# Performance work log

Hardware: AMD Instinct MI355X
Metric: run time of the kernel (lower is better)

## Reference

```python
import jax, jax.numpy as jnp
import numpy as np

B, T, D, H, MLP, WIN = 4, 2048, 768, 12, 3072, 256
HD = D // H


def setup_inputs() -> dict:
    key = jax.random.key(0)
    ks = jax.random.split(key, 9)
    s = 0.02
    return {
        "x": jax.random.normal(ks[0], (B, T, D), jnp.float32),
        "in_proj_w": jax.random.normal(ks[1], (3 * D, D), jnp.float32) * s,
        "in_proj_b": jax.random.normal(ks[2], (3 * D,), jnp.float32) * s,
        "out_w": jax.random.normal(ks[3], (D, D), jnp.float32) * s,
        "out_b": jax.random.normal(ks[4], (D,), jnp.float32) * s,
        "w1": jax.random.normal(ks[5], (MLP, D), jnp.float32) * s,
        "b1": jax.random.normal(ks[6], (MLP,), jnp.float32) * s,
        "w2": jax.random.normal(ks[7], (D, MLP), jnp.float32) * s,
        "b2": jax.random.normal(ks[8], (D,), jnp.float32) * s,
        "ln1_g": jnp.ones((D,), jnp.float32),
        "ln1_b": jnp.zeros((D,), jnp.float32),
        "ln2_g": jnp.ones((D,), jnp.float32),
        "ln2_b": jnp.zeros((D,), jnp.float32),
        "window_size": WIN,
    }


def _layernorm(v, g, b, eps=1e-5):
    m = v.mean(-1, keepdims=True)
    var = ((v - m) ** 2).mean(-1, keepdims=True)
    return (v - m) / jnp.sqrt(var + eps) * g + b


def reference(x, in_proj_w, in_proj_b, out_w, out_b, w1, b1, w2, b2,
              ln1_g, ln1_b, ln2_g, ln2_b, window_size):
    Bx, Tx, Dx = x.shape
    # --- local (banded) multi-head self-attention on norm1(x) ---
    xn = _layernorm(x, ln1_g, ln1_b)
    qkv = xn @ in_proj_w.T + in_proj_b            # [B,T,3D]
    q, k, v = jnp.split(qkv, 3, axis=-1)
    to_heads = lambda t: t.reshape(Bx, Tx, H, HD).transpose(0, 2, 1, 3)  # [B,H,T,hd]
    q, k, v = to_heads(q), to_heads(k), to_heads(v)
    scale = jnp.asarray(1.0 / np.sqrt(HD), x.dtype)
    scores = jnp.einsum('bhqd,bhkd->bhqk', q, k) * scale  # [B,H,T,T]
    idx = jnp.arange(Tx)
    banned = jnp.abs(idx[:, None] - idx[None, :]) > window_size  # True = masked
    scores = jnp.where(banned, -jnp.inf, scores)
    attn = jax.nn.softmax(scores, axis=-1)
    o = jnp.einsum('bhqk,bhkd->bhqd', attn, v)
    o = o.transpose(0, 2, 1, 3).reshape(Bx, Tx, Dx)
    o = o @ out_w.T + out_b
    x = x + o
    # --- MLP block on norm2(x) ---
    xn = _layernorm(x, ln2_g, ln2_b)
    h = jax.nn.gelu(xn @ w1.T + b1, approximate=False)
    x = x + (h @ w2.T + b2)
    return x
```

## Files before the change

### kernel.cpp

```cpp
#include <hip/hip_runtime.h>
#include <hip/hip_bf16.h>

typedef __bf16 bf16;
typedef __bf16 v8bf __attribute__((ext_vector_type(8)));
typedef __bf16 v4bf __attribute__((ext_vector_type(4)));
typedef float  v4f  __attribute__((ext_vector_type(4)));

#define DEVI __device__ __forceinline__

constexpr int Bc   = 4;
constexpr int Tc   = 2048;
constexpr int Dc   = 768;
constexpr int Hc   = 12;
constexpr int HDc  = 64;
constexpr int MLPc = 3072;
constexpr int QKVc = 2304;
constexpr int BTc  = Bc * Tc;

DEVI float b2f(bf16 x) { return (float)x; }
DEVI bf16  f2b(float x) { return (bf16)x; }

#define GLDS(gp, lp) __builtin_amdgcn_global_load_lds( \
    (const __attribute__((address_space(1))) void*)(gp), \
    (__attribute__((address_space(3))) void*)(lp), 16, 0, 0)

__global__ __launch_bounds__(256) void cvt2_kernel(
    const float* __restrict__ s0, bf16* __restrict__ d0, int n0,
    const float* __restrict__ s1, bf16* __restrict__ d1)
{
    int i = blockIdx.x * 256 + threadIdx.x;
    const float* s; bf16* d; int j;
    if (i < n0) { s = s0; d = d0; j = i; }
    else        { s = s1; d = d1; j = i - n0; }
    float4 v = ((const float4*)s)[j];
    v4bf o = { f2b(v.x), f2b(v.y), f2b(v.z), f2b(v.w) };
    ((v4bf*)d)[j] = o;
}

__global__ __launch_bounds__(256) void ln_kernel(
    const float* __restrict__ x, const float* __restrict__ g,
    const float* __restrict__ bt, bf16* __restrict__ out)
{
    const int row = blockIdx.x;
    const int t = threadIdx.x;
    const float* xr = x + (size_t)row * Dc;
    float v[3];
    v[0] = xr[t];
    v[1] = xr[t + 256];
    v[2] = xr[t + 512];
    float s = v[0] + v[1] + v[2];
    float s2 = v[0]*v[0] + v[1]*v[1] + v[2]*v[2];
    #pragma unroll
    for (int off = 32; off > 0; off >>= 1) {
        s  += __shfl_down(s, off);
        s2 += __shfl_down(s2, off);
    }
    __shared__ float red[8];
    const int wave = t >> 6, lane = t & 63;
    if (lane == 0) { red[wave] = s; red[4 + wave] = s2; }
    __syncthreads();
    s  = red[0] + red[1] + red[2] + red[3];
    s2 = red[4] + red[5] + red[6] + red[7];
    const float mean = s * (1.0f / Dc);
    const float var  = s2 * (1.0f / Dc) - mean * mean;
    const float rstd = rsqrtf(var + 1e-5f);
    bf16* orow = out + (size_t)row * Dc;
    #pragma unroll
    for (int i = 0; i < 3; i++) {
        int c = t + i * 256;
        orow[c] = f2b((v[i] - mean) * rstd * g[c] + bt[c]);
    }
}

enum { EPI_QKV = 0, EPI_GELU_BF16 = 1, EPI_RESID_F32 = 2, EPI_ACC_F32 = 3 };

template <int EPI, int TN>
__global__ __launch_bounds__(256) void gemm_bt(
    const bf16* __restrict__ A, const bf16* __restrict__ Bw,
    const float* __restrict__ bias,
    bf16* __restrict__ Cb, float* __restrict__ Cf,
    const float* __restrict__ resf,
    int M, int N, int K, int lda, int ldb)
{
    constexpr int MI = (TN == 128) ? 4 : 2;
    __shared__ __align__(16) bf16 sA[128 * 64];
    __shared__ __align__(16) bf16 sB[TN * 64];
    const int t = threadIdx.x, wave = t >> 6, lane = t & 63;
    const int moff = (TN == 128) ? (wave & 1) * 64 : wave * 32;
    const int noff = (TN == 128) ? (wave >> 1) * 64 : 0;
    const int nx = gridDim.x, ny = gridDim.y;
    const int bid = blockIdx.y * nx + blockIdx.x;
    const int xcd = bid & 7, kk = bid >> 3;
    const int m0 = (xcd * (ny >> 3) + kk / nx) * 128;
    const int n0 = (kk % nx) * TN;
    const bf16* Ag = A + (size_t)m0 * lda;
    const bf16* Bg = Bw + (size_t)n0 * ldb;

    v4f acc[MI][4];
    #pragma unroll
    for (int i = 0; i < MI; i++)
        #pragma unroll
        for (int j = 0; j < 4; j++) acc[i][j] = (v4f)(0.0f);

    for (int k0 = 0; k0 < K; k0 += 64) {
        #pragma unroll
        for (int i = 0; i < 4; i++) {
            int c = i * 256 + t;
            int r = c >> 3, j = (c & 7) ^ (r & 7);
            GLDS(Ag + (size_t)r * lda + k0 + j * 8,
                 &sA[(i * 256 + wave * 64) * 8]);
        }
        #pragma unroll
        for (int i = 0; i < TN / 32; i++) {
            int c = i * 256 + t;
            int r = c >> 3, j = (c & 7) ^ (r & 7);
            GLDS(Bg + (size_t)r * ldb + k0 + j * 8,
                 &sB[(i * 256 + wave * 64) * 8]);
        }
        __syncthreads();
        #pragma unroll
        for (int ks = 0; ks < 2; ks++) {
            const int rq = lane >> 4, rl = lane & 15;
            v8bf a[MI], b[4];
            #pragma unroll
            for (int mi = 0; mi < MI; mi++) {
                const int row = moff + mi * 16 + rl;
                a[mi] = *(const v8bf*)&sA[row * 64 + ((ks * 4 + rq) ^ (row & 7)) * 8];
            }
            #pragma unroll
            for (int ni = 0; ni < 4; ni++) {
                const int row = noff + ni * 16 + rl;
                b[ni] = *(const v8bf*)&sB[row * 64 + ((ks * 4 + rq) ^ (row & 7)) * 8];
            }
            #pragma unroll
            for (int mi = 0; mi < MI; mi++)
                #pragma unroll
                for (int ni = 0; ni < 4; ni++)
                    acc[mi][ni] = __builtin_amdgcn_mfma_f32_16x16x32_bf16(
                        a[mi], b[ni], acc[mi][ni], 0, 0, 0);
        }
        __syncthreads();
    }

    const int rq = lane >> 4, cn = lane & 15;
    #pragma unroll
    for (int mi = 0; mi < MI; mi++)
        #pragma unroll
        for (int ni = 0; ni < 4; ni++) {
            const int col = n0 + noff + ni * 16 + cn;
            const float bv = bias ? bias[col] : 0.0f;
            if constexpr (EPI == EPI_QKV) {
                const int row0 = m0 + moff + mi * 16 + rq * 4;
                if (n0 < 2 * Dc) {
                    bf16* dst = Cb + (col < Dc ? 0 : (size_t)BTc * Dc);
                    const int cadj = col < Dc ? col : col - Dc;
                    const float qs = (col < Dc) ? 0.18033688011112042f : 1.0f;
                    #pragma unroll
                    for (int r = 0; r < 4; r++)
                        dst[(size_t)(row0 + r) * Dc + cadj] = f2b((acc[mi][ni][r] + bv) * qs);
                } else {
                    const int vcol = col - 2 * Dc;
                    const int hh = vcol >> 6, hd = vcol & 63;
                    const int bb = row0 >> 11, t0 = row0 & 2047;
                    v4bf pk;
                    #pragma unroll
                    for (int r = 0; r < 4; r++) pk[r] = f2b(acc[mi][ni][r] + bv);
                    *(v4bf*)(Cb + 2 * (size_t)BTc * Dc +
                             (((size_t)bb * Hc + hh) * HDc + hd) * Tc + t0) = pk;
                }
            } else {
                #pragma unroll
                for (int r = 0; r < 4; r++) {
                    const int row = m0 + moff + mi * 16 + rq * 4 + r;
                    const size_t idx = (size_t)row * N + col;
                    float vv = acc[mi][ni][r] + bv;
                    if constexpr (EPI == EPI_GELU_BF16) {
                        Cb[idx] = f2b(0.5f * vv * (1.0f + erff(vv * 0.70710678118f)));
                    } else if constexpr (EPI == EPI_RESID_F32) {
                        Cf[idx] = vv + resf[idx];
                    } else {
                        Cf[idx] = vv + Cf[idx];
                    }
                }
            }
        }
}

__global__ __launch_bounds__(256, 3) void attn_kernel(
    const bf16* __restrict__ Qb, const bf16* __restrict__ Kb,
    const bf16* __restrict__ Vt, bf16* __restrict__ o,
    const int* __restrict__ winp)
{
    const int bh = blockIdx.x, qt = blockIdx.y;
    const int b = bh / Hc, h = bh % Hc;
    const int win = *winp;
    const int t = threadIdx.x, wave = t >> 6, lane = t & 63;
    const int rq = lane >> 4, cn = lane & 15;
    const int qw0 = qt * 128 + wave * 32;

    __shared__ __align__(16) bf16 sP[4][32 * 64];
    bf16* const sPw = &sP[wave][0];
    const int swz = (cn & 7) << 1;

    const bf16* qp  = Qb + ((size_t)b * Tc) * Dc + h * HDc;
    const bf16* kp  = Kb + ((size_t)b * Tc) * Dc + h * HDc;
    const bf16* vtp = Vt + (size_t)bh * HDc * Tc;

    v8bf qf[2][2];
    #pragma unroll
    for (int ks = 0; ks < 2; ks++)
        #pragma unroll
        for (int mi = 0; mi < 2; mi++)
            qf[ks][mi] = *(const v8bf*)(qp + (size_t)(qw0 + mi * 16 + cn) * Dc
                                        + ks * 32 + rq * 8);

    v4f acc_o[2][4];
    #pragma unroll
    for (int mi = 0; mi < 2; mi++)
        #pragma unroll
        for (int nh = 0; nh < 4; nh++) acc_o[mi][nh] = (v4f)(0.0f);
    float l_part[2] = {0.0f, 0.0f};

    const int k_lo = max(0, qw0 - win);
    const int k_hi = min(Tc - 1, qw0 + 31 + win);
    int kb0 = k_lo & ~63;

    v8bf kf[2][4];
    #pragma unroll
    for (int ks = 0; ks < 2; ks++)
        #pragma unroll
        for (int kb = 0; kb < 4; kb++)
            kf[ks][kb] = *(const v8bf*)(kp + (size_t)(kb0 + kb * 16 + cn) * Dc
                                        + ks * 32 + rq * 8);

    for (; kb0 <= k_hi; kb0 += 64) {
        v4f sf[4][2];
        #pragma unroll
        for (int kb = 0; kb < 4; kb++)
            #pragma unroll
            for (int mi = 0; mi < 2; mi++) sf[kb][mi] = (v4f)(0.0f);
        #pragma unroll
        for (int ks = 0; ks < 2; ks++)
            #pragma unroll
            for (int kb = 0; kb < 4; kb++)
                #pragma unroll
                for (int mi = 0; mi < 2; mi++)
                    sf[kb][mi] = __builtin_amdgcn_mfma_f32_16x16x32_bf16(
                        kf[ks][kb], qf[ks][mi], sf[kb][mi], 0, 0, 0);

        v8bf vf[2][4];
        #pragma unroll
        for (int ks = 0; ks < 2; ks++)
            #pragma unroll
            for (int nh = 0; nh < 4; nh++)
                vf[ks][nh] = *(const v8bf*)(vtp + (size_t)(nh * 16 + cn) * Tc
                                            + kb0 + ks * 32 + rq * 8);

        const bool need_mask = (kb0 + 63 - qw0 > win) || (qw0 + 31 - kb0 > win);
        #pragma unroll
        for (int kb = 0; kb < 4; kb++)
            #pragma unroll
            for (int mi = 0; mi < 2; mi++) {
                v4bf pk;
                #pragma unroll
                for (int r = 0; r < 4; r++) {
                    float tt = sf[kb][mi][r];
                    if (need_mask) {
                        int ki = kb0 + kb * 16 + rq * 4 + r;
                        int qi = qw0 + mi * 16 + cn;
                        int dd = qi - ki; dd = dd < 0 ? -dd : dd;
                        tt = (dd > win) ? -INFINITY : tt;
                    }
                    float p = exp2f(fminf(tt, 30.0f));
                    l_part[mi] += p;
                    pk[r] = f2b(p);
                }
                *(v4bf*)&sPw[(mi * 16 + cn) * 64 + (((kb * 4 + rq) ^ swz) << 2)] = pk;
            }

        {
            const int nkb = (kb0 + 64 <= k_hi) ? kb0 + 64 : kb0;
            #pragma unroll
            for (int ks = 0; ks < 2; ks++)
                #pragma unroll
                for (int kb = 0; kb < 4; kb++)
                    kf[ks][kb] = *(const v8bf*)(kp + (size_t)(nkb + kb * 16 + cn) * Dc
                                                + ks * 32 + rq * 8);
        }

        #pragma unroll
        for (int ks = 0; ks < 2; ks++) {
            v8bf pa[2];
            #pragma unroll
            for (int mi = 0; mi < 2; mi++)
                pa[mi] = *(const v8bf*)&sPw[(mi * 16 + cn) * 64
                                            + (((ks * 8 + rq * 2) ^ swz) << 2)];
            #pragma unroll
            for (int mi = 0; mi < 2; mi++)
                #pragma unroll
                for (int nh = 0; nh < 4; nh++)
                    acc_o[mi][nh] = __builtin_amdgcn_mfma_f32_16x16x32_bf16(
                        pa[mi], vf[ks][nh], acc_o[mi][nh], 0, 0, 0);
        }
    }

    #pragma unroll
    for (int mi = 0; mi < 2; mi++) {
        l_part[mi] += __shfl_xor(l_part[mi], 16);
        l_part[mi] += __shfl_xor(l_part[mi], 32);
    }

    bf16* ob = o + ((size_t)b * Tc + qw0) * Dc + h * HDc;
    #pragma unroll
    for (int mi = 0; mi < 2; mi++)
        #pragma unroll
        for (int r = 0; r < 4; r++) {
            const float lv = __shfl(l_part[mi], rq * 4 + r);
            const float invl = 1.0f / lv;
            #pragma unroll
            for (int nh = 0; nh < 4; nh++)
                ob[(size_t)(mi * 16 + rq * 4 + r) * Dc + nh * 16 + cn] =
                    f2b(acc_o[mi][nh][r] * invl);
        }
}

extern "C" void kernel_launch(void* const* d_in, const int* in_sizes, int n_in,
                              void* d_out, int out_size, void* d_ws, size_t ws_size,
                              hipStream_t stream)
{
    const float* x     = (const float*)d_in[0];
    const float* inw   = (const float*)d_in[1];
    const float* inb   = (const float*)d_in[2];
    const float* outw  = (const float*)d_in[3];
    const float* outb  = (const float*)d_in[4];
    const float* w1    = (const float*)d_in[5];
    const float* b1    = (const float*)d_in[6];
    const float* w2    = (const float*)d_in[7];
    const float* b2    = (const float*)d_in[8];
    const float* ln1g  = (const float*)d_in[9];
    const float* ln1b  = (const float*)d_in[10];
    const float* ln2g  = (const float*)d_in[11];
    const float* ln2b  = (const float*)d_in[12];
    const int*   winp  = (const int*)d_in[13];
    float* out = (float*)d_out;

    char* ws = (char*)d_ws;
    constexpr size_t A_OFF   = 0;
    constexpr size_t QKV_OFF = (size_t)BTc * Dc * 2;
    constexpr size_t WA_OFF  = QKV_OFF + 3 * (size_t)BTc * Dc * 2;
    constexpr size_t WS_NEED = WA_OFF + (size_t)(QKVc + Dc) * Dc * 2;
    if (ws_size < WS_NEED) return;

    bf16*  xn     = (bf16*)(ws + A_OFF);
    bf16*  qkvb   = (bf16*)(ws + QKV_OFF);
    bf16*  Qb     = qkvb;
    bf16*  Kb     = qkvb + (size_t)BTc * Dc;
    bf16*  Vt     = qkvb + 2 * (size_t)BTc * Dc;
    bf16*  hbuf   = (bf16*)(ws + QKV_OFF);
    bf16*  wmlp   = (bf16*)(ws + QKV_OFF + (size_t)BTc * (2 * Dc) * 2);
    bf16*  w1_b   = wmlp;
    bf16*  w2_b   = wmlp + (size_t)MLPc * Dc;
    bf16*  wqkv_b = (bf16*)(ws + WA_OFF);
    bf16*  wout_b = wqkv_b + (size_t)QKVc * Dc;

    constexpr int HALF = MLPc / 2;
    constexpr int NQKV4 = QKVc * Dc / 4, NOUT4 = Dc * Dc / 4;
    constexpr int NW14  = MLPc * Dc / 4, NW24  = Dc * MLPc / 4;

    cvt2_kernel<<<(NQKV4 + NOUT4) / 256, 256, 0, stream>>>(
        inw, wqkv_b, NQKV4, outw, wout_b);

    ln_kernel<<<BTc, 256, 0, stream>>>(x, ln1g, ln1b, xn);
    gemm_bt<EPI_QKV, 128><<<dim3(QKVc / 128, BTc / 128), 256, 0, stream>>>(
        xn, wqkv_b, inb, qkvb, nullptr, nullptr, BTc, QKVc, Dc, Dc, Dc);
    attn_kernel<<<dim3(Bc * Hc, Tc / 128), 256, 0, stream>>>(Qb, Kb, Vt, xn, winp);
    cvt2_kernel<<<(NW14 + NW24) / 256, 256, 0, stream>>>(
        w1, w1_b, NW14, w2, w2_b);
    gemm_bt<EPI_RESID_F32, 64><<<dim3(Dc / 64, BTc / 128), 256, 0, stream>>>(
        xn, wout_b, outb, nullptr, out, x, BTc, Dc, Dc, Dc, Dc);
    ln_kernel<<<BTc, 256, 0, stream>>>(out, ln2g, ln2b, xn);

    for (int c = 0; c < 2; c++) {
        const bf16* w1c = w1_b + (size_t)c * HALF * Dc;
        const bf16* w2c = w2_b + (size_t)c * HALF;
        gemm_bt<EPI_GELU_BF16, 128><<<dim3(HALF / 128, BTc / 128), 256, 0, stream>>>(
            xn, w1c, b1 + c * HALF, hbuf, nullptr, nullptr, BTc, HALF, Dc, Dc, Dc);
        gemm_bt<EPI_ACC_F32, 64><<<dim3(Dc / 64, BTc / 128), 256, 0, stream>>>(
            hbuf, w2c, (c == 0) ? b2 : nullptr, nullptr, out, nullptr,
            BTc, Dc, HALF, HALF, MLPc);
    }
}
```

Measured before the change: 382.0 us.

## Stage shared K/V tiles in LDS across the four waves of an attention block

The attention kernel used to have each wave load its own K and V fragments straight from global memory, with K prefetched in registers. Now the whole block walks the union of the four waves' key windows in 64-key tiles. Each tile of K and V is loaded once into swizzled LDS with direct global-to-LDS loads, and all waves read it from there. Waves skip the compute for tiles outside their own window. This cuts redundant global and L2 traffic, but adds two barriers per tile, removes the register prefetch overlap, adds 16KB of LDS per block, and makes some waves idle on edge tiles.

```diff
diff --git a/kernel.cpp b/kernel.cpp
--- a/kernel.cpp
+++ b/kernel.cpp
@@ -193,11 +193,14 @@
 {
     const int bh = blockIdx.x, qt = blockIdx.y;
     const int b = bh / Hc, h = bh % Hc;
+    const int q0 = qt * 128;
     const int win = *winp;
     const int t = threadIdx.x, wave = t >> 6, lane = t & 63;
     const int rq = lane >> 4, cn = lane & 15;
-    const int qw0 = qt * 128 + wave * 32;
-
+    const int qw0 = q0 + wave * 32;
+
+    __shared__ __align__(16) bf16 sK[64 * 64];
+    __shared__ __align__(16) bf16 sV[64 * 64];
     __shared__ __align__(16) bf16 sP[4][32 * 64];
     bf16* const sPw = &sP[wave][0];
     const int swz = (cn & 7) << 1;
@@ -221,87 +224,90 @@
         for (int nh = 0; nh < 4; nh++) acc_o[mi][nh] = (v4f)(0.0f);
     float l_part[2] = {0.0f, 0.0f};
 
-    const int k_lo = max(0, qw0 - win);
-    const int k_hi = min(Tc - 1, qw0 + 31 + win);
-    int kb0 = k_lo & ~63;
-
-    v8bf kf[2][4];
-    #pragma unroll
-    for (int ks = 0; ks < 2; ks++)
-        #pragma unroll
-        for (int kb = 0; kb < 4; kb++)
-            kf[ks][kb] = *(const v8bf*)(kp + (size_t)(kb0 + kb * 16 + cn) * Dc
-                                        + ks * 32 + rq * 8);
-
-    for (; kb0 <= k_hi; kb0 += 64) {
-        v4f sf[4][2];
-        #pragma unroll
-        for (int kb = 0; kb < 4; kb++)
-            #pragma unroll
-            for (int mi = 0; mi < 2; mi++) sf[kb][mi] = (v4f)(0.0f);
-        #pragma unroll
-        for (int ks = 0; ks < 2; ks++)
+    const int wlo = max(0, qw0 - win), whi = min(Tc - 1, qw0 + 31 + win);
+    const int klo = max(0, q0 - win) & ~63;
+    const int khi = min(Tc - 1, q0 + 127 + win);
+
+    for (int kb0 = klo; kb0 <= khi; kb0 += 64) {
+        #pragma unroll
+        for (int i = 0; i < 2; i++) {
+            int c = i * 256 + t;
+            int r = c >> 3, j = (c & 7) ^ (r & 7);
+            GLDS(kp + (size_t)(kb0 + r) * Dc + j * 8,
+                 &sK[(i * 256 + wave * 64) * 8]);
+            GLDS(vtp + (size_t)r * Tc + kb0 + j * 8,
+                 &sV[(i * 256 + wave * 64) * 8]);
+        }
+        __syncthreads();
+
+        if (kb0 + 63 >= wlo && kb0 <= whi) {
+            v4f sf[4][2];
             #pragma unroll
             for (int kb = 0; kb < 4; kb++)
                 #pragma unroll
+                for (int mi = 0; mi < 2; mi++) sf[kb][mi] = (v4f)(0.0f);
+            #pragma unroll
+            for (int ks = 0; ks < 2; ks++) {
+                v8bf kf[4];
+                #pragma unroll
+                for (int kb = 0; kb < 4; kb++) {
+                    const int row = kb * 16 + cn;
+                    kf[kb] = *(const v8bf*)&sK[row * 64
+                                              + ((ks * 4 + rq) ^ (row & 7)) * 8];
+                }
+                #pragma unroll
+                for (int kb = 0; kb < 4; kb++)
+                    #pragma unroll
+                    for (int mi = 0; mi < 2; mi++)
+                        sf[kb][mi] = __builtin_amdgcn_mfma_f32_16x16x32_bf16(
+                            kf[kb], qf[ks][mi], sf[kb][mi], 0, 0, 0);
+            }
+
+            const bool need_mask = (kb0 + 63 - qw0 > win) || (qw0 + 31 - kb0 > win);
+            #pragma unroll
+            for (int kb = 0; kb < 4; kb++)
+                #pragma unroll
+                for (int mi = 0; mi < 2; mi++) {
+                    v4bf pk;
+                    #pragma unroll
+                    for (int r = 0; r < 4; r++) {
+                        float tt = sf[kb][mi][r];
+                        if (need_mask) {
+                            int ki = kb0 + kb * 16 + rq * 4 + r;
+                            int qi = qw0 + mi * 16 + cn;
+                            int dd = qi - ki; dd = dd < 0 ? -dd : dd;
+                            tt = (dd > win) ? -INFINITY : tt;
+                        }
+                        float p = exp2f(fminf(tt, 30.0f));
+                        l_part[mi] += p;
+                        pk[r] = f2b(p);
+                    }
+                    *(v4bf*)&sPw[(mi * 16 + cn) * 64
+                                 + (((kb * 4 + rq) ^ swz) << 2)] = pk;
+                }
+
+            #pragma unroll
+            for (int ks = 0; ks < 2; ks++) {
+                v8bf pa[2], vf[4];
+                #pragma unroll
                 for (int mi = 0; mi < 2; mi++)
-                    sf[kb][mi] = __builtin_amdgcn_mfma_f32_16x16x32_bf16(
-                        kf[ks][kb], qf[ks][mi], sf[kb][mi], 0, 0, 0);
-
-        v8bf vf[2][4];
-        #pragma unroll
-        for (int ks = 0; ks < 2; ks++)
-            #pragma unroll
-            for (int nh = 0; nh < 4; nh++)
-                vf[ks][nh] = *(const v8bf*)(vtp + (size_t)(nh * 16 + cn) * Tc
-                                            + kb0 + ks * 32 + rq * 8);
-
-        const bool need_mask = (kb0 + 63 - qw0 > win) || (qw0 + 31 - kb0 > win);
-        #pragma unroll
-        for (int kb = 0; kb < 4; kb++)
-            #pragma unroll
-            for (int mi = 0; mi < 2; mi++) {
-                v4bf pk;
-                #pragma unroll
-                for (int r = 0; r < 4; r++) {
-                    float tt = sf[kb][mi][r];
-                    if (need_mask) {
-                        int ki = kb0 + kb * 16 + rq * 4 + r;
-                        int qi = qw0 + mi * 16 + cn;
-                        int dd = qi - ki; dd = dd < 0 ? -dd : dd;
-                        tt = (dd > win) ? -INFINITY : tt;
-                    }
-                    float p = exp2f(fminf(tt, 30.0f));
-                    l_part[mi] += p;
-                    pk[r] = f2b(p);
-                }
-                *(v4bf*)&sPw[(mi * 16 + cn) * 64 + (((kb * 4 + rq) ^ swz) << 2)] = pk;
-            }
-
-        {
-            const int nkb = (kb0 + 64 <= k_hi) ? kb0 + 64 : kb0;
-            #pragma unroll
-            for (int ks = 0; ks < 2; ks++)
-                #pragma unroll
-                for (int kb = 0; kb < 4; kb++)
-                    kf[ks][kb] = *(const v8bf*)(kp + (size_t)(nkb + kb * 16 + cn) * Dc
-                                                + ks * 32 + rq * 8);
-        }
-
-        #pragma unroll
-        for (int ks = 0; ks < 2; ks++) {
-            v8bf pa[2];
-            #pragma unroll
-            for (int mi = 0; mi < 2; mi++)
-                pa[mi] = *(const v8bf*)&sPw[(mi * 16 + cn) * 64
-                                            + (((ks * 8 + rq * 2) ^ swz) << 2)];
-            #pragma unroll
-            for (int mi = 0; mi < 2; mi++)
-                #pragma unroll
-                for (int nh = 0; nh < 4; nh++)
-                    acc_o[mi][nh] = __builtin_amdgcn_mfma_f32_16x16x32_bf16(
-                        pa[mi], vf[ks][nh], acc_o[mi][nh], 0, 0, 0);
-        }
+                    pa[mi] = *(const v8bf*)&sPw[(mi * 16 + cn) * 64
+                                                + (((ks * 8 + rq * 2) ^ swz) << 2)];
+                #pragma unroll
+                for (int nh = 0; nh < 4; nh++) {
+                    const int row = nh * 16 + cn;
+                    vf[nh] = *(const v8bf*)&sV[row * 64
+                                               + ((ks * 4 + rq) ^ (row & 7)) * 8];
+                }
+                #pragma unroll
+                for (int mi = 0; mi < 2; mi++)
+                    #pragma unroll
+                    for (int nh = 0; nh < 4; nh++)
+                        acc_o[mi][nh] = __builtin_amdgcn_mfma_f32_16x16x32_bf16(
+                            pa[mi], vf[ks * 0 + nh], acc_o[mi][nh], 0, 0, 0);
+            }
+        }
+        __syncthreads();
     }
 
     #pragma unroll
```

New measurement: 375.4 us. No clear change (-1.7%).
